# Performance work log

Hardware: AMD Instinct MI355X
Metric: run time of the kernel (lower is better)

## Reference

```python
import jax, jax.numpy as jnp
import numpy as np

C, H, V, N, T = 256, 256, 10000, 8, 256


def _residual_mlp(x, w1, b1, w2, b2, w3, b3):
    # ResidualLayerOld: relu(lin2(relu(lin1(x)))) + x, then final Linear
    h = jax.nn.relu(x @ w1 + b1)
    h = jax.nn.relu(h @ w2 + b2) + x
    return h @ w3 + b3


def setup_inputs() -> dict:
    key = jax.random.key(0)
    ks = jax.random.split(key, 16)
    p = lambda k, shape: jax.random.normal(k, shape, jnp.float32) * 0.02
    return dict(
        text=jax.random.randint(ks[0], (N, T), 0, V),
        mask=jnp.ones((N, T), dtype=bool),
        lengths=jnp.full((N,), T - 1, dtype=jnp.int32),  # full-length sequences
        start_emb=jax.random.normal(ks[1], (C, H), jnp.float32),
        state_emb=jax.random.normal(ks[2], (C, H), jnp.float32),
        preterminal_emb=jax.random.normal(ks[3], (C, H), jnp.float32),
        start_w1=p(ks[4], (H, H)), start_b1=jnp.zeros((H,), jnp.float32),
        start_w2=p(ks[5], (H, H)), start_b2=jnp.zeros((H,), jnp.float32),
        start_w3=p(ks[6], (H, 1)), start_b3=jnp.zeros((1,), jnp.float32),
        trans_w1=p(ks[7], (H, H)), trans_b1=jnp.zeros((H,), jnp.float32),
        trans_w2=p(ks[8], (H, H)), trans_b2=jnp.zeros((H,), jnp.float32),
        trans_w3=p(ks[9], (H, C)), trans_b3=jnp.zeros((C,), jnp.float32),
        term_w1=p(ks[10], (H, H)), term_b1=jnp.zeros((H,), jnp.float32),
        term_w2=p(ks[11], (H, H)), term_b2=jnp.zeros((H,), jnp.float32),
        term_w3=p(ks[12], (H, V)), term_b3=jnp.zeros((V,), jnp.float32),
    )


def _score(text, mask, lengths,
           start_emb, state_emb, preterminal_emb,
           start_w1, start_b1, start_w2, start_b2, start_w3, start_b3,
           trans_w1, trans_b1, trans_w2, trans_b2, trans_w3, trans_b3,
           term_w1, term_b1, term_w2, term_b2, term_w3, term_b3):
    n, t = text.shape
    c = state_emb.shape[0]
    # start / transition / emission distributions (dropout_type == 'none')
    init = jax.nn.log_softmax(
        _residual_mlp(start_emb, start_w1, start_b1, start_w2, start_b2, start_w3, start_b3)[:, 0], -1)  # [C]
    trans = jax.nn.log_softmax(
        _residual_mlp(state_emb, trans_w1, trans_b1, trans_w2, trans_b2, trans_w3, trans_b3), -1)  # [C,C]
    log_em = jax.nn.log_softmax(
        _residual_mlp(preterminal_emb, term_w1, term_b1, term_w2, term_b2, term_w3, term_b3), -1)  # [C,V]
    obs = log_em.T[text]  # [N,T,C], log p(x_t | z=c)
    # torch_struct LinearChain.hmm edge potentials: phi[n,t,c_next,c_prev]
    phi = trans[None, None] + obs[:, 1:, :, None]  # [N,T-1,C,C]
    phi = phi.at[:, 0].add(init[None, None, :] + obs[:, 0][:, None, :])
    phi_t = jnp.swapaxes(phi, 0, 1)  # [T-1,N,C,C]

    def fwd_step(alpha, p):
        new = jax.nn.logsumexp(p + alpha[:, None, :], axis=-1)  # reduce over c_prev
        return new, new

    _, alphas = jax.lax.scan(fwd_step, jnp.zeros((n, c), phi.dtype), phi_t)  # [T-1,N,C]

    def bwd_step(beta, p):
        new = jax.nn.logsumexp(p + beta[:, :, None], axis=1)  # reduce over c_next
        return new, beta

    _, betas = jax.lax.scan(bwd_step, jnp.zeros((n, c), phi.dtype), phi_t, reverse=True)  # [T-1,N,C]

    alpha_prev = jnp.concatenate([jnp.zeros((1, n, c), phi.dtype), alphas[:-1]], 0)
    log_Z = jax.nn.logsumexp(alphas[-1], -1)  # [N]
    # edge posteriors
    log_m = alpha_prev[:, :, None, :] + phi_t + betas[:, :, :, None] - log_Z[None, :, None, None]
    marginals = jnp.swapaxes(jnp.exp(log_m), 0, 1)  # [N,T-1,C,C]

    evidence = jax.nn.logsumexp(alphas[lengths - 1, jnp.arange(n)], -1).sum()
    elbo = jnp.where(mask[:, 1:, None, None],
                     jax.lax.stop_gradient(marginals) * phi,
                     0.0).sum()
    return elbo, evidence


def reference(text, mask, lengths,
              start_emb, state_emb, preterminal_emb,
              start_w1, start_b1, start_w2, start_b2, start_w3, start_b3,
              trans_w1, trans_b1, trans_w2, trans_b2, trans_w3, trans_b3,
              term_w1, term_b1, term_w2, term_b2, term_w3, term_b3):
    elbo, evidence = _score(text, mask, lengths,
                            start_emb, state_emb, preterminal_emb,
                            start_w1, start_b1, start_w2, start_b2, start_w3, start_b3,
                            trans_w1, trans_b1, trans_w2, trans_b2, trans_w3, trans_b3,
                            term_w1, term_b1, term_w2, term_b2, term_w3, term_b3)
    return elbo, evidence
```

## Files before the change

### kernel.cpp

```cpp
#include <hip/hip_runtime.h>
#include <hip/hip_bf16.h>

#define C_ 256
#define H_ 256
#define V_ 10000
#define N_ 8
#define T_ 256
#define TM1_ 255
#define NB_ ((V_ + 31) / 32)
#define SW_ 8

typedef _Float16 h2_t __attribute__((ext_vector_type(2)));
typedef _Float16 h4_t __attribute__((ext_vector_type(4)));
typedef _Float16 h8_t __attribute__((ext_vector_type(8)));
typedef float f4v __attribute__((ext_vector_type(4)));

__device__ __forceinline__ void bar_lgkm() {
  asm volatile("s_waitcnt lgkmcnt(0)\ns_barrier" ::: "memory");
}

__device__ __forceinline__ float wave_red_max(float v) {
#define DPP_MAX(ctrl) { int iv_ = __float_as_int(v); \
  int r_ = __builtin_amdgcn_update_dpp(iv_, iv_, ctrl, 0xF, 0xF, false); \
  v = fmaxf(v, __int_as_float(r_)); }
  DPP_MAX(0x111) DPP_MAX(0x112) DPP_MAX(0x114) DPP_MAX(0x118)
  DPP_MAX(0x142) DPP_MAX(0x143)
#undef DPP_MAX
  return __int_as_float(__builtin_amdgcn_readlane(__float_as_int(v), 63));
}
__device__ __forceinline__ float wave_red_sum(float v) {
#define DPP_ADD(ctrl) { \
  int r_ = __builtin_amdgcn_update_dpp(0, __float_as_int(v), ctrl, 0xF, 0xF, true); \
  v += __int_as_float(r_); }
  DPP_ADD(0x111) DPP_ADD(0x112) DPP_ADD(0x114) DPP_ADD(0x118)
  DPP_ADD(0x142) DPP_ADD(0x143)
#undef DPP_ADD
  return __int_as_float(__builtin_amdgcn_readlane(__float_as_int(v), 63));
}

__device__ __forceinline__ float block_allmax(float v, float* red) {
  v = wave_red_max(v);
  if ((threadIdx.x & 63) == 0) red[threadIdx.x >> 6] = v;
  __syncthreads();
  v = fmaxf(fmaxf(red[0], red[1]), fmaxf(red[2], red[3]));
  __syncthreads();
  return v;
}
__device__ __forceinline__ float block_allsum(float v, float* red) {
  v = wave_red_sum(v);
  if ((threadIdx.x & 63) == 0) red[threadIdx.x >> 6] = v;
  __syncthreads();
  v = (red[0] + red[1]) + (red[2] + red[3]);
  __syncthreads();
  return v;
}

__device__ __forceinline__ void mlp4(
    const float* __restrict__ emb,
    const float* __restrict__ w1, const float* __restrict__ b1,
    const float* __restrict__ w2, const float* __restrict__ b2,
    int r0, float (&e_s)[4][C_], float (&h_s)[4][C_], float (&h2_s)[4][C_]) {
  const int tid = threadIdx.x;
#pragma unroll
  for (int rr = 0; rr < 4; ++rr)
    e_s[rr][tid] = emb[(r0 + rr) * H_ + tid];
  __syncthreads();
  float bb = b1[tid];
  float a0 = bb, a1 = bb, a2 = bb, a3 = bb;
  for (int k4 = 0; k4 < H_ / 4; ++k4) {
    float4 e0 = ((const float4*)e_s[0])[k4];
    float4 e1 = ((const float4*)e_s[1])[k4];
    float4 e2 = ((const float4*)e_s[2])[k4];
    float4 e3 = ((const float4*)e_s[3])[k4];
    const float* wp = w1 + (k4 * 4) * H_ + tid;
    float wa = wp[0], wb = wp[H_], wc = wp[2 * H_], wd = wp[3 * H_];
    a0 = fmaf(e0.x, wa, a0); a0 = fmaf(e0.y, wb, a0);
    a0 = fmaf(e0.z, wc, a0); a0 = fmaf(e0.w, wd, a0);
    a1 = fmaf(e1.x, wa, a1); a1 = fmaf(e1.y, wb, a1);
    a1 = fmaf(e1.z, wc, a1); a1 = fmaf(e1.w, wd, a1);
    a2 = fmaf(e2.x, wa, a2); a2 = fmaf(e2.y, wb, a2);
    a2 = fmaf(e2.z, wc, a2); a2 = fmaf(e2.w, wd, a2);
    a3 = fmaf(e3.x, wa, a3); a3 = fmaf(e3.y, wb, a3);
    a3 = fmaf(e3.z, wc, a3); a3 = fmaf(e3.w, wd, a3);
  }
  h_s[0][tid] = fmaxf(a0, 0.f);
  h_s[1][tid] = fmaxf(a1, 0.f);
  h_s[2][tid] = fmaxf(a2, 0.f);
  h_s[3][tid] = fmaxf(a3, 0.f);
  __syncthreads();
  bb = b2[tid];
  a0 = bb; a1 = bb; a2 = bb; a3 = bb;
  for (int k4 = 0; k4 < H_ / 4; ++k4) {
    float4 e0 = ((const float4*)h_s[0])[k4];
    float4 e1 = ((const float4*)h_s[1])[k4];
    float4 e2 = ((const float4*)h_s[2])[k4];
    float4 e3 = ((const float4*)h_s[3])[k4];
    const float* wp = w2 + (k4 * 4) * H_ + tid;
    float wa = wp[0], wb = wp[H_], wc = wp[2 * H_], wd = wp[3 * H_];
    a0 = fmaf(e0.x, wa, a0); a0 = fmaf(e0.y, wb, a0);
    a0 = fmaf(e0.z, wc, a0); a0 = fmaf(e0.w, wd, a0);
    a1 = fmaf(e1.x, wa, a1); a1 = fmaf(e1.y, wb, a1);
    a1 = fmaf(e1.z, wc, a1); a1 = fmaf(e1.w, wd, a1);
    a2 = fmaf(e2.x, wa, a2); a2 = fmaf(e2.y, wb, a2);
    a2 = fmaf(e2.z, wc, a2); a2 = fmaf(e2.w, wd, a2);
    a3 = fmaf(e3.x, wa, a3); a3 = fmaf(e3.y, wb, a3);
    a3 = fmaf(e3.z, wc, a3); a3 = fmaf(e3.w, wd, a3);
  }
  h2_s[0][tid] = fmaxf(a0, 0.f) + e_s[0][tid];
  h2_s[1][tid] = fmaxf(a1, 0.f) + e_s[1][tid];
  h2_s[2][tid] = fmaxf(a2, 0.f) + e_s[2][tid];
  h2_s[3][tid] = fmaxf(a3, 0.f) + e_s[3][tid];
  __syncthreads();
}

__global__ __launch_bounds__(256) void k_heads(
    const float* __restrict__ semb, const float* __restrict__ sw1,
    const float* __restrict__ sb1, const float* __restrict__ sw2,
    const float* __restrict__ sb2, const float* __restrict__ sw3,
    const float* __restrict__ sb3, float* __restrict__ slogit,
    const float* __restrict__ temb, const float* __restrict__ tw1,
    const float* __restrict__ tb1, const float* __restrict__ tw2,
    const float* __restrict__ tb2, const float* __restrict__ tw3,
    const float* __restrict__ tb3, float* __restrict__ Pf,
    float* __restrict__ PLf, float* __restrict__ PTf,
    _Float16* __restrict__ P_h, _Float16* __restrict__ PT_h,
    const float* __restrict__ eemb, const float* __restrict__ ew1,
    const float* __restrict__ eb1, const float* __restrict__ ew2,
    const float* __restrict__ eb2, float* __restrict__ H2,
    float* __restrict__ H2T) {
  __shared__ __align__(16) float e_s[4][C_], h_s[4][C_], h2_s[4][C_];
  __shared__ float red[4];
  const int b = blockIdx.x;
  const int tid = threadIdx.x;
  if (b < 64) {
    const int r0 = b * 4;
    mlp4(semb, sw1, sb1, sw2, sb2, r0, e_s, h_s, h2_s);
    float w3v = sw3[tid];
    float s0 = block_allsum(h2_s[0][tid] * w3v, red);
    float s1 = block_allsum(h2_s[1][tid] * w3v, red);
    float s2 = block_allsum(h2_s[2][tid] * w3v, red);
    float s3 = block_allsum(h2_s[3][tid] * w3v, red);
    if (tid == 0) {
      float bb = sb3[0];
      slogit[r0 + 0] = s0 + bb;
      slogit[r0 + 1] = s1 + bb;
      slogit[r0 + 2] = s2 + bb;
      slogit[r0 + 3] = s3 + bb;
    }
  } else if (b < 128) {
    const int r0 = (b - 64) * 4;
    mlp4(temb, tw1, tb1, tw2, tb2, r0, e_s, h_s, h2_s);
    float lb = tb3[tid];
    float l0 = lb, l1 = lb, l2 = lb, l3 = lb;
    for (int k4 = 0; k4 < H_ / 4; ++k4) {
      float4 e0 = ((const float4*)h2_s[0])[k4];
      float4 e1 = ((const float4*)h2_s[1])[k4];
      float4 e2 = ((const float4*)h2_s[2])[k4];
      float4 e3 = ((const float4*)h2_s[3])[k4];
      const float* wp = tw3 + (k4 * 4) * C_ + tid;
      float wa = wp[0], wb = wp[C_], wc = wp[2 * C_], wd = wp[3 * C_];
      l0 = fmaf(e0.x, wa, l0); l0 = fmaf(e0.y, wb, l0);
      l0 = fmaf(e0.z, wc, l0); l0 = fmaf(e0.w, wd, l0);
      l1 = fmaf(e1.x, wa, l1); l1 = fmaf(e1.y, wb, l1);
      l1 = fmaf(e1.z, wc, l1); l1 = fmaf(e1.w, wd, l1);
      l2 = fmaf(e2.x, wa, l2); l2 = fmaf(e2.y, wb, l2);
      l2 = fmaf(e2.z, wc, l2); l2 = fmaf(e2.w, wd, l2);
      l3 = fmaf(e3.x, wa, l3); l3 = fmaf(e3.y, wb, l3);
      l3 = fmaf(e3.z, wc, l3); l3 = fmaf(e3.w, wd, l3);
    }
    float lg[4] = {l0, l1, l2, l3};
#pragma unroll
    for (int rr = 0; rr < 4; ++rr) {
      float m = block_allmax(lg[rr], red);
      float e = __expf(lg[rr] - m);
      float se = block_allsum(e, red);
      float p = e / se;
      float tv = lg[rr] - m - __logf(se);
      const int r = r0 + rr;
      Pf[r * C_ + tid] = p;
      PLf[r * C_ + tid] = p * tv;
      PTf[tid * C_ + r] = p;
      P_h[r * C_ + tid] = (_Float16)p;
      PT_h[tid * C_ + r] = (_Float16)p;
    }
  } else {
    const int r0 = (b - 128) * 4;
    mlp4(eemb, ew1, eb1, ew2, eb2, r0, e_s, h_s, h2_s);
#pragma unroll
    for (int rr = 0; rr < 4; ++rr) {
      const int r = r0 + rr;
      float v = h2_s[rr][tid];
      H2[r * H_ + tid] = v;
      H2T[tid * C_ + r] = v;
    }
  }
}

__global__ __launch_bounds__(256) void k_term_stats(
    const float* __restrict__ H2, const float* __restrict__ w3,
    const float* __restrict__ b3, float* __restrict__ partm,
    float* __restrict__ parts) {
  __shared__ __align__(16) float w3_s[H_][32];
  __shared__ float b3_s[32];
  const int v0 = blockIdx.x * 32;
  const int tid = threadIdx.x;
  const int ncols = min(32, V_ - v0);
  for (int idx = tid; idx < H_ * 32; idx += 256) {
    int k = idx >> 5, c = idx & 31;
    w3_s[k][c] = (c < ncols) ? w3[k * V_ + v0 + c] : 0.f;
  }
  if (tid < 32) b3_s[tid] = (tid < ncols) ? b3[v0 + tid] : 0.f;
  __syncthreads();
  float acc[32];
#pragma unroll
  for (int c = 0; c < 32; ++c) acc[c] = 0.f;
  const float4* hq = (const float4*)(H2 + tid * H_);
  for (int k4 = 0; k4 < H_ / 4; ++k4) {
    float4 h = hq[k4];
    float hk[4];
    *(float4*)hk = h;
#pragma unroll
    for (int kk = 0; kk < 4; ++kk) {
      float hv = hk[kk];
      const int k = k4 * 4 + kk;
      const float4* wq = (const float4*)(&w3_s[k][0]);
#pragma unroll
      for (int c4 = 0; c4 < 8; ++c4) {
        float4 w = wq[c4];
        acc[c4 * 4 + 0] = fmaf(hv, w.x, acc[c4 * 4 + 0]);
        acc[c4 * 4 + 1] = fmaf(hv, w.y, acc[c4 * 4 + 1]);
        acc[c4 * 4 + 2] = fmaf(hv, w.z, acc[c4 * 4 + 2]);
        acc[c4 * 4 + 3] = fmaf(hv, w.w, acc[c4 * 4 + 3]);
      }
    }
  }
  float m = -1e30f;
#pragma unroll
  for (int c = 0; c < 32; ++c) {
    acc[c] += b3_s[c];
    if (c < ncols) m = fmaxf(m, acc[c]);
  }
  float se = 0.f;
#pragma unroll
  for (int c = 0; c < 32; ++c)
    if (c < ncols) se += __expf(acc[c] - m);
  partm[blockIdx.x * C_ + tid] = m;
  parts[blockIdx.x * C_ + tid] = se;
}

__global__ void k_small(const float* __restrict__ slogit,
                        float* __restrict__ initv,
                        const float* __restrict__ partm,
                        const float* __restrict__ parts,
                        float* __restrict__ denom) {
  __shared__ float red[4];
  const int tid = threadIdx.x;
  if (blockIdx.x == 0) {
    float x = slogit[tid];
    float m = block_allmax(x, red);
    float se = block_allsum(__expf(x - m), red);
    initv[tid] = x - m - __logf(se);
  } else {
    const int r = tid;
    float m = -1e30f;
    for (int b = 0; b < NB_; ++b) m = fmaxf(m, partm[b * C_ + r]);
    float s = 0.f;
    for (int b = 0; b < NB_; ++b)
      s += parts[b * C_ + r] * __expf(partm[b * C_ + r] - m);
    denom[r] = m + __logf(s);
  }
}

__global__ __launch_bounds__(256) void k_obs2(
    const int* __restrict__ text, const float* __restrict__ H2T,
    const float* __restrict__ w3, const float* __restrict__ b3,
    const float* __restrict__ denom, float* __restrict__ EOBS,
    float* __restrict__ Karr) {
  __shared__ __align__(16) float w_s[H_][8];
  __shared__ float redm[4][8];
  const int c = threadIdx.x;
  const int wid = c >> 6;
  const int lane = c & 63;
  const int base = blockIdx.x * 8;
  int tok[8];
#pragma unroll
  for (int i = 0; i < 8; ++i) tok[i] = text[base + i];
  float wtmp[8];
#pragma unroll
  for (int i = 0; i < 8; ++i) wtmp[i] = w3[c * V_ + tok[i]];
  float b3t[8];
#pragma unroll
  for (int i = 0; i < 8; ++i) b3t[i] = b3[tok[i]];
#pragma unroll
  for (int i = 0; i < 8; ++i) w_s[c][i] = wtmp[i];
  __syncthreads();
  float acc[8];
#pragma unroll
  for (int i = 0; i < 8; ++i) acc[i] = 0.f;
  for (int k4 = 0; k4 < H_ / 4; ++k4) {
    float hv[4];
#pragma unroll
    for (int kk = 0; kk < 4; ++kk) hv[kk] = H2T[(k4 * 4 + kk) * C_ + c];
#pragma unroll
    for (int kk = 0; kk < 4; ++kk) {
      const float4* wq = (const float4*)(&w_s[k4 * 4 + kk][0]);
      float4 wa = wq[0], wb = wq[1];
      acc[0] = fmaf(hv[kk], wa.x, acc[0]);
      acc[1] = fmaf(hv[kk], wa.y, acc[1]);
      acc[2] = fmaf(hv[kk], wa.z, acc[2]);
      acc[3] = fmaf(hv[kk], wa.w, acc[3]);
      acc[4] = fmaf(hv[kk], wb.x, acc[4]);
      acc[5] = fmaf(hv[kk], wb.y, acc[5]);
      acc[6] = fmaf(hv[kk], wb.z, acc[6]);
      acc[7] = fmaf(hv[kk], wb.w, acc[7]);
    }
  }
  float dn = denom[c];
  float obsv[8];
#pragma unroll
  for (int i = 0; i < 8; ++i) obsv[i] = acc[i] + b3t[i] - dn;
#pragma unroll
  for (int i = 0; i < 8; ++i) {
    float wm = wave_red_max(obsv[i]);
    if (lane == 0) redm[wid][i] = wm;
  }
  __syncthreads();
#pragma unroll
  for (int i = 0; i < 8; ++i) {
    float Ki = fmaxf(fmaxf(redm[0][i], redm[1][i]),
                     fmaxf(redm[2][i], redm[3][i]));
    EOBS[(base + i) * C_ + c] = __expf(obsv[i] - Ki);
    if (c == 0) Karr[base + i] = Ki;
  }
}

__global__ __launch_bounds__(512, 2) void k_scan6(
    const _Float16* __restrict__ P_h, const _Float16* __restrict__ PT_h,
    const float* __restrict__ initv, const float* __restrict__ EOBS,
    const float* __restrict__ Karr, float* __restrict__ AL,
    float* __restrict__ BL, float* __restrict__ CC, float* __restrict__ DD,
    float* __restrict__ KT, float* __restrict__ LOGZ) {
  __shared__ __align__(16) _Float16 ubuf[2][C_];
  __shared__ __align__(16) float red[SW_];
  const int tid = threadIdx.x;
  const int w = tid >> 6;
  const int lane = tid & 63;
  const int quad = lane >> 4;
  const int nn16 = lane & 15;
  const bool bwd = blockIdx.x >= N_;
  const int n = blockIdx.x & (N_ - 1);
  const _Float16* __restrict__ M = bwd ? PT_h : P_h;

  h8_t afrag[2][8];
#pragma unroll
  for (int m = 0; m < 2; ++m) {
    const _Float16* rp = M + (size_t)((w << 5) + (m << 4) + nn16) * C_ + (quad << 3);
#pragma unroll
    for (int kt = 0; kt < 8; ++kt)
      afrag[m][kt] = *(const h8_t*)(rp + (kt << 5));
  }
  const int stb = (w << 5) + (quad << 2);
  const float* __restrict__ eob = EOBS + (size_t)n * T_ * C_;
  int cur = 0;

  f4v eoA[2], eoB[2], eoC[2];
#define FLOAD(SL, tt) { \
  eo##SL[0] = *(const f4v*)(eob + (size_t)(tt) * C_ + stb); \
  eo##SL[1] = *(const f4v*)(eob + (size_t)(tt) * C_ + stb + 16); }

  if (!bwd) {
    float kvp = (tid >= 1 && tid < 256) ? Karr[n * T_ + tid] : 0.f;
    kvp = wave_red_sum(kvp);
    if (lane == 0) red[w] = kvp;
    __syncthreads();
    float KPtot = ((red[0] + red[1]) + (red[2] + red[3])) +
                  ((red[4] + red[5]) + (red[6] + red[7]));
    if (tid == 0) KT[n] = KPtot;
    __syncthreads();

    float K0 = Karr[n * T_];
    f4v x0[2];
    float lmax = -1e30f;
#pragma unroll
    for (int m = 0; m < 2; ++m) {
      const int st0 = stb + (m << 4);
      f4v iv = *(const f4v*)(initv + st0);
      f4v e0 = *(const f4v*)(eob + st0);
#pragma unroll
      for (int r = 0; r < 4; ++r) {
        x0[m][r] = iv[r] + __logf(e0[r]) + K0;
        lmax = fmaxf(lmax, x0[m][r]);
      }
    }
    float wmx = wave_red_max(lmax);
    if (lane == 0) red[w] = wmx;
    __syncthreads();
    f4v rr0 = *(const f4v*)&red[0];
    f4v rr1 = *(const f4v*)&red[4];
    float m0 = fmaxf(fmaxf(fmaxf(rr0[0], rr0[1]), fmaxf(rr0[2], rr0[3])),
                     fmaxf(fmaxf(rr1[0], rr1[1]), fmaxf(rr1[2], rr1[3])));
    __syncthreads();
    float CLacc = m0;
    f4v uval[2];
#pragma unroll
    for (int m = 0; m < 2; ++m) {
      const int st0 = stb + (m << 4);
#pragma unroll
      for (int r = 0; r < 4; ++r) uval[m][r] = __expf(x0[m][r] - m0);
      if (nn16 == 0) {
        h4_t p;
#pragma unroll
        for (int r = 0; r < 4; ++r) p[r] = (_Float16)uval[m][r];
        *(h4_t*)(&ubuf[0][st0]) = p;
        *(f4v*)(AL + (size_t)(0 * N_ + n) * C_ + st0) = uval[m];
      }
    }
    if (tid == 0) CC[0 * N_ + n] = CLacc;
    float invm = 1.f, logm = 0.f;
    FLOAD(B, 1)
    FLOAD(C, 2)
    __syncthreads();

#define FSTEP(tt, SL, SC) do { \
    if ((tt) + 3 < T_) FLOAD(SL, (tt) + 3) \
    const _Float16* ubc = &ubuf[cur][0]; \
    _Float16* ubn = &ubuf[cur ^ 1][0]; \
    h8_t bf[8]; \
    _Pragma("unroll") for (int kt = 0; kt < 8; ++kt) \
      bf[kt] = *(const h8_t*)(ubc + (kt << 5) + (quad << 3)); \
    f4v acc0 = (f4v){0.f, 0.f, 0.f, 0.f}; \
    f4v acc1 = (f4v){0.f, 0.f, 0.f, 0.f}; \
    _Pragma("unroll") for (int kt = 0; kt < 8; ++kt) { \
      acc0 = __builtin_amdgcn_mfma_f32_16x16x32_f16(afrag[0][kt], bf[kt], acc0, 0, 0, 0); \
      acc1 = __builtin_amdgcn_mfma_f32_16x16x32_f16(afrag[1][kt], bf[kt], acc1, 0, 0, 0); } \
    float lmx = -1e30f; \
    _Pragma("unroll") for (int r = 0; r < 4; ++r) { \
      uval[0][r] = acc0[r] * invm * eo##SC[0][r]; lmx = fmaxf(lmx, uval[0][r]); \
      uval[1][r] = acc1[r] * invm * eo##SC[1][r]; lmx = fmaxf(lmx, uval[1][r]); } \
    CLacc += logm; \
    const bool resc_ = ((tt) & 3) == 3; \
    if (resc_) { \
      float wmm = wave_red_max(lmx); \
      if (lane == 0) red[w] = wmm; } \
    if (nn16 == 0) { \
      _Pragma("unroll") for (int m = 0; m < 2; ++m) { \
        const int st0 = stb + (m << 4); \
        h4_t p; \
        _Pragma("unroll") for (int r = 0; r < 4; ++r) p[r] = (_Float16)uval[m][r]; \
        *(h4_t*)(ubn + st0) = p; \
        *(f4v*)(AL + (size_t)(((tt) + 1) * N_ + n) * C_ + st0) = uval[m]; } } \
    if (tid == 0) CC[((tt) + 1) * N_ + n] = CLacc; \
    bar_lgkm(); \
    if (resc_) { \
      f4v q0 = *(const f4v*)&red[0]; \
      f4v q1 = *(const f4v*)&red[4]; \
      float mm = fmaxf(fmaxf(fmaxf(q0[0], q0[1]), fmaxf(q0[2], q0[3])), \
                       fmaxf(fmaxf(q1[0], q1[1]), fmaxf(q1[2], q1[3]))); \
      mm = fmaxf(mm, 1e-30f); \
      invm = 1.f / mm; \
      logm = __logf(mm); \
    } else { invm = 1.f; logm = 0.f; } \
    cur ^= 1; \
  } while (0)

#pragma unroll 1
    for (int tb = 0; tb < TM1_; tb += 3) {
      FSTEP(tb + 0, A, B);
      FSTEP(tb + 1, B, C);
      FSTEP(tb + 2, C, A);
    }
#undef FSTEP
    float s = 0.f;
#pragma unroll
    for (int m = 0; m < 2; ++m)
      s += (uval[m][0] + uval[m][1]) + (uval[m][2] + uval[m][3]);
    s = wave_red_sum(s);
    if (lane == 0) red[w] = s;
    __syncthreads();
    if (tid == 0) {
      float S = ((red[0] + red[1]) + (red[2] + red[3])) +
                ((red[4] + red[5]) + (red[6] + red[7]));
      LOGZ[n] = __logf(S * (1.f / 16.f)) + CLacc + KPtot;
    }
  } else {
    float DLacc = 0.f;
    f4v vval[2];
#pragma unroll
    for (int m = 0; m < 2; ++m) {
      const int st0 = stb + (m << 4);
      vval[m] = *(const f4v*)(eob + (size_t)TM1_ * C_ + st0);
      if (nn16 == 0) {
        h4_t p;
#pragma unroll
        for (int r = 0; r < 4; ++r) p[r] = (_Float16)vval[m][r];
        *(h4_t*)(&ubuf[0][st0]) = p;
        f4v one = (f4v){1.f, 1.f, 1.f, 1.f};
        *(f4v*)(BL + (size_t)((TM1_ - 1) * N_ + n) * C_ + st0) = one;
      }
    }
    if (tid == 0) DD[(TM1_ - 1) * N_ + n] = 0.f;
    FLOAD(B, TM1_ - 1)
    FLOAD(C, TM1_ - 2)
    __syncthreads();

#define BSTEP(itv, SL, SC) do { \
    if ((itv) < TM1_ - 1) { \
      const int t_ = TM1_ - 2 - (itv); \
      if ((itv) <= TM1_ - 4) FLOAD(SL, t_ - 1) \
      float invm = 1.f, logm = 0.f; \
      if (((itv) & 3) == 3) { \
        f4v q0 = *(const f4v*)&red[0]; \
        f4v q1 = *(const f4v*)&red[4]; \
        float mm = fmaxf(fmaxf(fmaxf(q0[0], q0[1]), fmaxf(q0[2], q0[3])), \
                         fmaxf(fmaxf(q1[0], q1[1]), fmaxf(q1[2], q1[3]))); \
        mm = fmaxf(mm, 1e-30f); \
        invm = 1.f / mm; \
        logm = __logf(mm); } \
      const _Float16* ubc = &ubuf[cur][0]; \
      _Float16* ubn = &ubuf[cur ^ 1][0]; \
      h8_t bf[8]; \
      _Pragma("unroll") for (int kt = 0; kt < 8; ++kt) \
        bf[kt] = *(const h8_t*)(ubc + (kt << 5) + (quad << 3)); \
      f4v acc0 = (f4v){0.f, 0.f, 0.f, 0.f}; \
      f4v acc1 = (f4v){0.f, 0.f, 0.f, 0.f}; \
      _Pragma("unroll") for (int kt = 0; kt < 8; ++kt) { \
        acc0 = __builtin_amdgcn_mfma_f32_16x16x32_f16(afrag[0][kt], bf[kt], acc0, 0, 0, 0); \
        acc1 = __builtin_amdgcn_mfma_f32_16x16x32_f16(afrag[1][kt], bf[kt], acc1, 0, 0, 0); } \
      DLacc += logm; \
      float lmx = -1e30f; \
      f4v blv[2]; \
      _Pragma("unroll") for (int r = 0; r < 4; ++r) { \
        blv[0][r] = acc0[r] * invm; \
        vval[0][r] = blv[0][r] * eo##SC[0][r]; lmx = fmaxf(lmx, vval[0][r]); \
        blv[1][r] = acc1[r] * invm; \
        vval[1][r] = blv[1][r] * eo##SC[1][r]; lmx = fmaxf(lmx, vval[1][r]); } \
      if ((((itv) + 1) & 3) == 3) { \
        float wmm = wave_red_max(lmx); \
        if (lane == 0) red[w] = wmm; } \
      if (nn16 == 0) { \
        _Pragma("unroll") for (int m = 0; m < 2; ++m) { \
          const int st0 = stb + (m << 4); \
          h4_t p; \
          _Pragma("unroll") for (int r = 0; r < 4; ++r) p[r] = (_Float16)vval[m][r]; \
          *(h4_t*)(ubn + st0) = p; \
          *(f4v*)(BL + (size_t)(t_ * N_ + n) * C_ + st0) = blv[m]; } } \
      if (tid == 0) DD[t_ * N_ + n] = DLacc; \
      bar_lgkm(); \
      cur ^= 1; \
    } \
  } while (0)

#pragma unroll 1
    for (int ib = 0; ib < 255; ib += 3) {
      BSTEP(ib + 0, A, B);
      BSTEP(ib + 1, B, C);
      BSTEP(ib + 2, C, A);
    }
#undef BSTEP
  }
#undef FLOAD
}

__global__ __launch_bounds__(256) void k_elbo(
    const float* __restrict__ Pf, const float* __restrict__ PLf,
    const float* __restrict__ PTf, const float* __restrict__ AL,
    const float* __restrict__ BL, const float* __restrict__ CC,
    const float* __restrict__ DD, const float* __restrict__ EOBS,
    const float* __restrict__ Karr, const float* __restrict__ KT,
    const float* __restrict__ LOGZ, float* __restrict__ out) {
  __shared__ __align__(16) float A_s[N_][C_];
  __shared__ __align__(16) float B_s[N_][C_];
  __shared__ float red[4];
  const int t = blockIdx.x;
  const int c = threadIdx.x;
  if (t == 0 && c == 0) {
    float s = 0.f;
#pragma unroll
    for (int nn = 0; nn < N_; ++nn) s += LOGZ[nn];
    out[1] = s;
  }
  float sc[N_], Kv[N_], cc[N_];
#pragma unroll
  for (int nn = 0; nn < N_; ++nn) {
    A_s[nn][c] = AL[(t * N_ + nn) * C_ + c];
    Kv[nn] = Karr[nn * T_ + t + 1];
    cc[nn] = CC[t * N_ + nn];
    sc[nn] = __expf(cc[nn] + DD[t * N_ + nn] + KT[nn] - LOGZ[nn]);
  }
  __syncthreads();
  float accPA[N_], accPL[N_];
#pragma unroll
  for (int nn = 0; nn < N_; ++nn) { accPA[nn] = 0.f; accPL[nn] = 0.f; }
  const float4* pr = (const float4*)(Pf + c * C_);
  const float4* plr = (const float4*)(PLf + c * C_);
  for (int j = 0; j < C_ / 4; ++j) {
    float4 p = pr[j];
    float4 pl = plr[j];
#pragma unroll
    for (int nn = 0; nn < N_; ++nn) {
      float4 a = ((const float4*)A_s[nn])[j];
      accPA[nn] += p.x * a.x + p.y * a.y + p.z * a.z + p.w * a.w;
      accPL[nn] += pl.x * a.x + pl.y * a.y + pl.z * a.z + pl.w * a.w;
    }
  }
  float contrib = 0.f;
  float Bv[N_];
#pragma unroll
  for (int nn = 0; nn < N_; ++nn) {
    float eo = EOBS[(nn * T_ + t + 1) * C_ + c];
    float ob = __logf(eo) + Kv[nn];
    float B = eo * BL[(t * N_ + nn) * C_ + c] * sc[nn];
    Bv[nn] = B;
    contrib += B * fmaf(ob, accPA[nn], accPL[nn]);
  }
  if (t == 0) {
#pragma unroll
    for (int nn = 0; nn < N_; ++nn) B_s[nn][c] = Bv[nn];
    __syncthreads();
    const float4* ptq = (const float4*)(PTf + c * C_);
    float accPT[N_];
#pragma unroll
    for (int nn = 0; nn < N_; ++nn) accPT[nn] = 0.f;
    for (int j = 0; j < C_ / 4; ++j) {
      float4 p = ptq[j];
#pragma unroll
      for (int nn = 0; nn < N_; ++nn) {
        float4 b = ((const float4*)B_s[nn])[j];
        accPT[nn] += p.x * b.x + p.y * b.y + p.z * b.z + p.w * b.w;
      }
    }
#pragma unroll
    for (int nn = 0; nn < N_; ++nn) {
      float a0v = A_s[nn][c];
      if (a0v > 0.f)
        contrib += a0v * (__logf(a0v) + cc[nn]) * accPT[nn];
    }
  }
  contrib = wave_red_sum(contrib);
  if ((c & 63) == 0) red[c >> 6] = contrib;
  __syncthreads();
  if (c == 0) atomicAdd(out, (red[0] + red[1]) + (red[2] + red[3]));
}

extern "C" void kernel_launch(void* const* d_in, const int* in_sizes, int n_in,
                              void* d_out, int out_size, void* d_ws, size_t ws_size,
                              hipStream_t stream) {
  (void)in_sizes; (void)n_in; (void)out_size; (void)ws_size;
  const int* text = (const int*)d_in[0];
  const float* start_emb = (const float*)d_in[3];
  const float* state_emb = (const float*)d_in[4];
  const float* pre_emb   = (const float*)d_in[5];
  const float* sw1 = (const float*)d_in[6];  const float* sb1 = (const float*)d_in[7];
  const float* sw2 = (const float*)d_in[8];  const float* sb2 = (const float*)d_in[9];
  const float* sw3 = (const float*)d_in[10]; const float* sb3 = (const float*)d_in[11];
  const float* tw1 = (const float*)d_in[12]; const float* tb1 = (const float*)d_in[13];
  const float* tw2 = (const float*)d_in[14]; const float* tb2 = (const float*)d_in[15];
  const float* tw3 = (const float*)d_in[16]; const float* tb3 = (const float*)d_in[17];
  const float* ew1 = (const float*)d_in[18]; const float* eb1 = (const float*)d_in[19];
  const float* ew2 = (const float*)d_in[20]; const float* eb2 = (const float*)d_in[21];
  const float* ew3 = (const float*)d_in[22]; const float* eb3 = (const float*)d_in[23];
  float* out = (float*)d_out;

  char* p = (char*)d_ws;
  auto alloc = [&](size_t bytes) -> char* {
    char* r = p;
    p += (bytes + 255) & ~(size_t)255;
    return r;
  };
  float* slogit = (float*)alloc(C_ * 4);
  float* initv  = (float*)alloc(C_ * 4);
  float* denom  = (float*)alloc(C_ * 4);
  float* LOGZ   = (float*)alloc(N_ * 4);
  float* KT     = (float*)alloc(N_ * 4);
  float* Pf     = (float*)alloc(C_ * C_ * 4);
  float* PLf    = (float*)alloc(C_ * C_ * 4);
  float* PTf    = (float*)alloc(C_ * C_ * 4);
  _Float16* P_h  = (_Float16*)alloc(C_ * C_ * 2);
  _Float16* PT_h = (_Float16*)alloc(C_ * C_ * 2);
  float* H2    = (float*)alloc(C_ * H_ * 4);
  float* H2T   = (float*)alloc(C_ * H_ * 4);
  float* partm = (float*)alloc(NB_ * C_ * 4);
  float* parts = (float*)alloc(NB_ * C_ * 4);
  float* EOBS  = (float*)alloc((size_t)N_ * T_ * C_ * 4);
  float* Karr  = (float*)alloc((size_t)N_ * T_ * 4);
  float* AL    = (float*)alloc((size_t)T_ * N_ * C_ * 4);
  float* BL    = (float*)alloc((size_t)TM1_ * N_ * C_ * 4);
  float* CC    = (float*)alloc((size_t)T_ * N_ * 4);
  float* DD    = (float*)alloc((size_t)TM1_ * N_ * 4);

  hipMemsetAsync(d_out, 0, 2 * sizeof(float), stream);

  k_heads<<<dim3(192), dim3(256), 0, stream>>>(
      start_emb, sw1, sb1, sw2, sb2, sw3, sb3, slogit,
      state_emb, tw1, tb1, tw2, tb2, tw3, tb3, Pf, PLf, PTf, P_h, PT_h,
      pre_emb, ew1, eb1, ew2, eb2, H2, H2T);
  k_term_stats<<<dim3(NB_), dim3(256), 0, stream>>>(H2, ew3, eb3, partm, parts);
  k_small<<<dim3(2), dim3(256), 0, stream>>>(slogit, initv, partm, parts, denom);
  k_obs2<<<dim3(N_ * T_ / 8), dim3(256), 0, stream>>>(text, H2T, ew3, eb3, denom, EOBS, Karr);
  k_scan6<<<dim3(2 * N_), dim3(512), 0, stream>>>(P_h, PT_h, initv, EOBS, Karr,
                                                  AL, BL, CC, DD, KT, LOGZ);
  k_elbo<<<dim3(TM1_), dim3(256), 0, stream>>>(Pf, PLf, PTf, AL, BL, CC, DD,
                                               EOBS, Karr, KT, LOGZ, out);
}
```

Measured before the change: 467.7 us.

## Fold k_small into consumers and deepen emission prefetch in scan

Removes the k_small launch. The emission-denominator reduction over partial stats moves into each k_obs2 block, and the initial log-softmax moves into the forward scan block. The scan's emission prefetch ring grows from 3 to 5 slots and each load is issued after the current step's use, to hide global-load latency in the serial recurrence. k_obs2 now redundantly reduces NB_ partials per block, and the deeper ring uses more registers.

```diff
diff --git a/kernel.cpp b/kernel.cpp
--- a/kernel.cpp
+++ b/kernel.cpp
@@ -248,34 +248,11 @@
   parts[blockIdx.x * C_ + tid] = se;
 }
 
-__global__ void k_small(const float* __restrict__ slogit,
-                        float* __restrict__ initv,
-                        const float* __restrict__ partm,
-                        const float* __restrict__ parts,
-                        float* __restrict__ denom) {
-  __shared__ float red[4];
-  const int tid = threadIdx.x;
-  if (blockIdx.x == 0) {
-    float x = slogit[tid];
-    float m = block_allmax(x, red);
-    float se = block_allsum(__expf(x - m), red);
-    initv[tid] = x - m - __logf(se);
-  } else {
-    const int r = tid;
-    float m = -1e30f;
-    for (int b = 0; b < NB_; ++b) m = fmaxf(m, partm[b * C_ + r]);
-    float s = 0.f;
-    for (int b = 0; b < NB_; ++b)
-      s += parts[b * C_ + r] * __expf(partm[b * C_ + r] - m);
-    denom[r] = m + __logf(s);
-  }
-}
-
 __global__ __launch_bounds__(256) void k_obs2(
     const int* __restrict__ text, const float* __restrict__ H2T,
     const float* __restrict__ w3, const float* __restrict__ b3,
-    const float* __restrict__ denom, float* __restrict__ EOBS,
-    float* __restrict__ Karr) {
+    const float* __restrict__ partm, const float* __restrict__ parts,
+    float* __restrict__ EOBS, float* __restrict__ Karr) {
   __shared__ __align__(16) float w_s[H_][8];
   __shared__ float redm[4][8];
   const int c = threadIdx.x;
@@ -291,6 +268,12 @@
   float b3t[8];
 #pragma unroll
   for (int i = 0; i < 8; ++i) b3t[i] = b3[tok[i]];
+  float dm = -1e30f;
+  for (int b = 0; b < NB_; ++b) dm = fmaxf(dm, partm[b * C_ + c]);
+  float ds = 0.f;
+  for (int b = 0; b < NB_; ++b)
+    ds += parts[b * C_ + c] * __expf(partm[b * C_ + c] - dm);
+  float dn = dm + __logf(ds);
 #pragma unroll
   for (int i = 0; i < 8; ++i) w_s[c][i] = wtmp[i];
   __syncthreads();
@@ -315,7 +298,6 @@
       acc[7] = fmaf(hv[kk], wb.w, acc[7]);
     }
   }
-  float dn = denom[c];
   float obsv[8];
 #pragma unroll
   for (int i = 0; i < 8; ++i) obsv[i] = acc[i] + b3t[i] - dn;
@@ -334,14 +316,15 @@
   }
 }
 
-__global__ __launch_bounds__(512, 2) void k_scan6(
+__global__ __launch_bounds__(512, 2) void k_scan7(
     const _Float16* __restrict__ P_h, const _Float16* __restrict__ PT_h,
-    const float* __restrict__ initv, const float* __restrict__ EOBS,
+    const float* __restrict__ slogit, const float* __restrict__ EOBS,
     const float* __restrict__ Karr, float* __restrict__ AL,
     float* __restrict__ BL, float* __restrict__ CC, float* __restrict__ DD,
     float* __restrict__ KT, float* __restrict__ LOGZ) {
   __shared__ __align__(16) _Float16 ubuf[2][C_];
   __shared__ __align__(16) float red[SW_];
+  __shared__ __align__(16) float initv_s[C_];
   const int tid = threadIdx.x;
   const int w = tid >> 6;
   const int lane = tid & 63;
@@ -363,10 +346,10 @@
   const float* __restrict__ eob = EOBS + (size_t)n * T_ * C_;
   int cur = 0;
 
-  f4v eoA[2], eoB[2], eoC[2];
-#define FLOAD(SL, tt) { \
-  eo##SL[0] = *(const f4v*)(eob + (size_t)(tt) * C_ + stb); \
-  eo##SL[1] = *(const f4v*)(eob + (size_t)(tt) * C_ + stb + 16); }
+  f4v eoS0[2], eoS1[2], eoS2[2], eoS3[2], eoS4[2];
+#define FLOAD(S, tt) { \
+  eoS##S[0] = *(const f4v*)(eob + (size_t)(tt) * C_ + stb); \
+  eoS##S[1] = *(const f4v*)(eob + (size_t)(tt) * C_ + stb + 16); }
 
   if (!bwd) {
     float kvp = (tid >= 1 && tid < 256) ? Karr[n * T_ + tid] : 0.f;
@@ -378,13 +361,29 @@
     if (tid == 0) KT[n] = KPtot;
     __syncthreads();
 
+    float xs = (tid < C_) ? slogit[tid] : -1e30f;
+    float wm0 = wave_red_max(xs);
+    if (lane == 0) red[w] = wm0;
+    __syncthreads();
+    float im = fmaxf(fmaxf(fmaxf(red[0], red[1]), fmaxf(red[2], red[3])),
+                     fmaxf(fmaxf(red[4], red[5]), fmaxf(red[6], red[7])));
+    __syncthreads();
+    float ex = (tid < C_) ? __expf(xs - im) : 0.f;
+    float ws0 = wave_red_sum(ex);
+    if (lane == 0) red[w] = ws0;
+    __syncthreads();
+    float ise = ((red[0] + red[1]) + (red[2] + red[3])) +
+                ((red[4] + red[5]) + (red[6] + red[7]));
+    if (tid < C_) initv_s[tid] = xs - im - __logf(ise);
+    __syncthreads();
+
     float K0 = Karr[n * T_];
     f4v x0[2];
     float lmax = -1e30f;
 #pragma unroll
     for (int m = 0; m < 2; ++m) {
       const int st0 = stb + (m << 4);
-      f4v iv = *(const f4v*)(initv + st0);
+      f4v iv = *(const f4v*)(initv_s + st0);
       f4v e0 = *(const f4v*)(eob + st0);
 #pragma unroll
       for (int r = 0; r < 4; ++r) {
@@ -417,12 +416,10 @@
     }
     if (tid == 0) CC[0 * N_ + n] = CLacc;
     float invm = 1.f, logm = 0.f;
-    FLOAD(B, 1)
-    FLOAD(C, 2)
-    __syncthreads();
-
-#define FSTEP(tt, SL, SC) do { \
-    if ((tt) + 3 < T_) FLOAD(SL, (tt) + 3) \
+    FLOAD(1, 1) FLOAD(2, 2) FLOAD(3, 3) FLOAD(4, 4) FLOAD(0, 5)
+    __syncthreads();
+
+#define FSTEP(tt, S) do { \
     const _Float16* ubc = &ubuf[cur][0]; \
     _Float16* ubn = &ubuf[cur ^ 1][0]; \
     h8_t bf[8]; \
@@ -435,8 +432,9 @@
       acc1 = __builtin_amdgcn_mfma_f32_16x16x32_f16(afrag[1][kt], bf[kt], acc1, 0, 0, 0); } \
     float lmx = -1e30f; \
     _Pragma("unroll") for (int r = 0; r < 4; ++r) { \
-      uval[0][r] = acc0[r] * invm * eo##SC[0][r]; lmx = fmaxf(lmx, uval[0][r]); \
-      uval[1][r] = acc1[r] * invm * eo##SC[1][r]; lmx = fmaxf(lmx, uval[1][r]); } \
+      uval[0][r] = acc0[r] * invm * eoS##S[0][r]; lmx = fmaxf(lmx, uval[0][r]); \
+      uval[1][r] = acc1[r] * invm * eoS##S[1][r]; lmx = fmaxf(lmx, uval[1][r]); } \
+    if ((tt) + 6 <= TM1_) FLOAD(S, (tt) + 6)    \
     CLacc += logm; \
     const bool resc_ = ((tt) & 3) == 3; \
     if (resc_) { \
@@ -464,10 +462,12 @@
   } while (0)
 
 #pragma unroll 1
-    for (int tb = 0; tb < TM1_; tb += 3) {
-      FSTEP(tb + 0, A, B);
-      FSTEP(tb + 1, B, C);
-      FSTEP(tb + 2, C, A);
+    for (int tb = 0; tb < TM1_; tb += 5) {
+      FSTEP(tb + 0, 1);
+      FSTEP(tb + 1, 2);
+      FSTEP(tb + 2, 3);
+      FSTEP(tb + 3, 4);
+      FSTEP(tb + 4, 0);
     }
 #undef FSTEP
     float s = 0.f;
@@ -499,14 +499,12 @@
       }
     }
     if (tid == 0) DD[(TM1_ - 1) * N_ + n] = 0.f;
-    FLOAD(B, TM1_ - 1)
-    FLOAD(C, TM1_ - 2)
-    __syncthreads();
-
-#define BSTEP(itv, SL, SC) do { \
-    if ((itv) < TM1_ - 1) { \
+    FLOAD(0, 254) FLOAD(1, 253) FLOAD(2, 252) FLOAD(3, 251) FLOAD(4, 250)
+    __syncthreads();
+
+#define BSTEP(itv, S) do { \
+    if ((itv) < 254) { \
       const int t_ = TM1_ - 2 - (itv); \
-      if ((itv) <= TM1_ - 4) FLOAD(SL, t_ - 1) \
       float invm = 1.f, logm = 0.f; \
       if (((itv) & 3) == 3) { \
         f4v q0 = *(const f4v*)&red[0]; \
@@ -531,9 +529,10 @@
       f4v blv[2]; \
       _Pragma("unroll") for (int r = 0; r < 4; ++r) { \
         blv[0][r] = acc0[r] * invm; \
-        vval[0][r] = blv[0][r] * eo##SC[0][r]; lmx = fmaxf(lmx, vval[0][r]); \
+        vval[0][r] = blv[0][r] * eoS##S[0][r]; lmx = fmaxf(lmx, vval[0][r]); \
         blv[1][r] = acc1[r] * invm; \
-        vval[1][r] = blv[1][r] * eo##SC[1][r]; lmx = fmaxf(lmx, vval[1][r]); } \
+        vval[1][r] = blv[1][r] * eoS##S[1][r]; lmx = fmaxf(lmx, vval[1][r]); } \
+      if ((itv) <= 249) FLOAD(S, 249 - (itv))    \
       if ((((itv) + 1) & 3) == 3) { \
         float wmm = wave_red_max(lmx); \
         if (lane == 0) red[w] = wmm; } \
@@ -551,10 +550,12 @@
   } while (0)
 
 #pragma unroll 1
-    for (int ib = 0; ib < 255; ib += 3) {
-      BSTEP(ib + 0, A, B);
-      BSTEP(ib + 1, B, C);
-      BSTEP(ib + 2, C, A);
+    for (int ib = 0; ib < 255; ib += 5) {
+      BSTEP(ib + 0, 0);
+      BSTEP(ib + 1, 1);
+      BSTEP(ib + 2, 2);
+      BSTEP(ib + 3, 3);
+      BSTEP(ib + 4, 4);
     }
 #undef BSTEP
   }
@@ -668,8 +669,6 @@
     return r;
   };
   float* slogit = (float*)alloc(C_ * 4);
-  float* initv  = (float*)alloc(C_ * 4);
-  float* denom  = (float*)alloc(C_ * 4);
   float* LOGZ   = (float*)alloc(N_ * 4);
   float* KT     = (float*)alloc(N_ * 4);
   float* Pf     = (float*)alloc(C_ * C_ * 4);
@@ -695,9 +694,9 @@
       state_emb, tw1, tb1, tw2, tb2, tw3, tb3, Pf, PLf, PTf, P_h, PT_h,
       pre_emb, ew1, eb1, ew2, eb2, H2, H2T);
   k_term_stats<<<dim3(NB_), dim3(256), 0, stream>>>(H2, ew3, eb3, partm, parts);
-  k_small<<<dim3(2), dim3(256), 0, stream>>>(slogit, initv, partm, parts, denom);
-  k_obs2<<<dim3(N_ * T_ / 8), dim3(256), 0, stream>>>(text, H2T, ew3, eb3, denom, EOBS, Karr);
-  k_scan6<<<dim3(2 * N_), dim3(512), 0, stream>>>(P_h, PT_h, initv, EOBS, Karr,
+  k_obs2<<<dim3(N_ * T_ / 8), dim3(256), 0, stream>>>(text, H2T, ew3, eb3,
+                                                      partm, parts, EOBS, Karr);
+  k_scan7<<<dim3(2 * N_), dim3(512), 0, stream>>>(P_h, PT_h, slogit, EOBS, Karr,
                                                   AL, BL, CC, DD, KT, LOGZ);
   k_elbo<<<dim3(TM1_), dim3(256), 0, stream>>>(Pf, PLf, PTf, AL, BL, CC, DD,
                                                EOBS, Karr, KT, LOGZ, out);
```

Result: no change. 476.9 us (+2.0%).
